# Performance work log

Hardware: AMD Instinct MI355X
Metric: run time of the kernel (lower is better)

Reference implementation:

```python
import jax, jax.numpy as jnp
import numpy as np

C_IN = 64
C_INT = 32

def conv1x1(x, w, b):
    # x: [B,C,H,W], w: [O,C], b: [O]
    return jnp.einsum('bchw,oc->bohw', x, w) + b[None, :, None, None]

def maxpool2(x):
    # 2x2 max pool, stride 2. x: [B,C,H,W]
    B, C, H, W = x.shape
    return x.reshape(B, C, H // 2, 2, W // 2, 2).max(axis=(3, 5))

def setup_inputs() -> dict:
    key = jax.random.key(0)
    ks = jax.random.split(key, 9)
    s = 1.0 / np.sqrt(C_IN)
    si = 1.0 / np.sqrt(C_INT)
    x = jax.random.normal(ks[0], (16, C_IN, 64, 64), dtype=jnp.float32)
    return {
        'x': x,
        'w_origin': jax.random.normal(ks[1], (C_INT, C_IN), dtype=jnp.float32) * s,
        'b_origin': jax.random.normal(ks[2], (C_INT,), dtype=jnp.float32) * s,
        'w_theta': jax.random.normal(ks[3], (C_INT, C_IN), dtype=jnp.float32) * s,
        'b_theta': jax.random.normal(ks[4], (C_INT,), dtype=jnp.float32) * s,
        'w_phi': jax.random.normal(ks[5], (C_INT, C_IN), dtype=jnp.float32) * s,
        'b_phi': jax.random.normal(ks[6], (C_INT,), dtype=jnp.float32) * s,
        'w_W': jax.random.normal(ks[7], (C_IN, C_INT), dtype=jnp.float32) * si,
        'b_W': jax.random.normal(ks[8], (C_IN,), dtype=jnp.float32) * si,
    }

def reference(x, w_origin, b_origin, w_theta, b_theta, w_phi, b_phi, w_W, b_W):
    B, C, H, W = x.shape
    # value: conv1x1 + maxpool -> [B, Ci, H/2, W/2] -> [B, Nkv, Ci]
    f_x = maxpool2(conv1x1(x, w_origin, b_origin))
    f_x = f_x.reshape(B, C_INT, -1).transpose(0, 2, 1)
    # query: conv1x1 (no pooling) -> [B, N, Ci]
    theta_x = conv1x1(x, w_theta, b_theta).reshape(B, C_INT, -1).transpose(0, 2, 1)
    # key: conv1x1 + maxpool -> [B, Ci, Nkv]
    phi_x = maxpool2(conv1x1(x, w_phi, b_phi)).reshape(B, C_INT, -1)
    # attention: [B, N, Nkv]
    f = jnp.einsum('bnc,bcm->bnm', theta_x, phi_x)
    f_div_C = jax.nn.softmax(f, axis=-1)
    y = jnp.einsum('bnm,bmc->bnc', f_div_C, f_x)  # [B, N, Ci]
    y = y.transpose(0, 2, 1).reshape(B, C_INT, H, W)
    z = conv1x1(y, w_W, b_W) + x
    return z
```

## Files before the change

### kernel.cpp

```cpp
#include <hip/hip_runtime.h>
#include <math.h>


#define B_SZ 16
#define HW 4096
#define NKV 1024
#define XSTR 65
#define YS 40
#define LOG2E 1.4426950408889634f

typedef __attribute__((ext_vector_type(8))) short bfrag;
typedef __attribute__((ext_vector_type(4))) short sfrag;
typedef __attribute__((ext_vector_type(4))) float f32x4;

static __device__ __forceinline__ ushort f2bf(float v) {
  union { float f; uint u; } c; c.f = v;
  uint b = c.u + 0x7FFFu + ((c.u >> 16) & 1u);
  return (ushort)(b >> 16);
}
static __device__ __forceinline__ float bf2f(ushort h) {
  union { uint u; float f; } c; c.u = (uint)h << 16; return c.f;
}
static __device__ __forceinline__ uint cvtpk(float a, float b) {
  uint r; asm("v_cvt_pk_bf16_f32 %0, %1, %2" : "=v"(r) : "v"(a), "v"(b));
  return r;
}
static __device__ __forceinline__ void split2(float a, float b, uint& h, uint& l) {
  h = cvtpk(a, b);
  float ha = __uint_as_float(h << 16);
  float hb = __uint_as_float(h & 0xFFFF0000u);
  l = cvtpk(a - ha, b - hb);
}

__global__ __launch_bounds__(256) void k_prep(
    const float* __restrict__ wt, const float* __restrict__ wp,
    const float* __restrict__ wo, const float* __restrict__ wW,
    ushort* __restrict__ WTH, ushort* __restrict__ WTL,
    ushort* __restrict__ WPH, ushort* __restrict__ WPL,
    ushort* __restrict__ WOH, ushort* __restrict__ WWH,
    ushort* __restrict__ WWL) {
  int t = threadIdx.x;
  int p = t >> 6, lane = t & 63, l15 = lane & 15, quad = lane >> 4;
  {
    int nt = p >> 1, kh2 = p & 1;
    const float* rt = wt + (size_t)(nt * 16 + l15) * 64 + kh2 * 32 + quad * 8;
    const float* rp = wp + (size_t)(nt * 16 + l15) * 64 + kh2 * 32 + quad * 8;
    const float* ro = wo + (size_t)(nt * 16 + l15) * 64 + kh2 * 32 + quad * 8;
    union { ushort u[8]; uint4 v; } th, tl, ph, pl, oh;
    #pragma unroll
    for (int j = 0; j < 8; ++j) {
      float v = rt[j] * LOG2E;
      ushort hb = f2bf(v);
      th.u[j] = hb; tl.u[j] = f2bf(v - bf2f(hb));
      v = rp[j]; hb = f2bf(v);
      ph.u[j] = hb; pl.u[j] = f2bf(v - bf2f(hb));
      oh.u[j] = f2bf(ro[j]);
    }
    size_t base = (size_t)t * 8;
    *(uint4*)(WTH + base) = th.v;
    *(uint4*)(WTL + base) = tl.v;
    *(uint4*)(WPH + base) = ph.v;
    *(uint4*)(WPL + base) = pl.v;
    *(uint4*)(WOH + base) = oh.v;
  }
  #pragma unroll
  for (int s = 0; s < 2; ++s) {
    int idx = s * 256 + t;
    int p2 = idx >> 6, ln = idx & 63;
    int fl = ln & 15, fq = ln >> 4;
    int wv = p2 >> 1, kt = p2 & 1;
    const float* rw = wW + (size_t)(wv * 16 + fl) * 32 + kt * 16 + fq * 4;
    union { ushort u[4]; uint2 v; } h, l;
    #pragma unroll
    for (int j = 0; j < 4; ++j) {
      float v = rw[j];
      ushort hb = f2bf(v);
      h.u[j] = hb; l.u[j] = f2bf(v - bf2f(hb));
    }
    *(uint2*)(WWH + (size_t)idx * 4) = h.v;
    *(uint2*)(WWL + (size_t)idx * 4) = l.v;
  }
}

__global__ __launch_bounds__(512) void k_qkv(
    const float* __restrict__ x,
    const ushort* __restrict__ WTH, const ushort* __restrict__ WTL,
    const float* __restrict__ bt,
    const ushort* __restrict__ WPH, const ushort* __restrict__ WPL,
    const float* __restrict__ bp,
    const ushort* __restrict__ WOH, const float* __restrict__ bo,
    ushort* __restrict__ QH, ushort* __restrict__ QL,
    ushort* __restrict__ KH, ushort* __restrict__ KL, ushort* __restrict__ VF) {
  __shared__ float sx[128 * XSTR];
  __shared__ float sPool[2][2][32][33];

  int t = threadIdx.x;
  int W = t >> 6, lane = t & 63, l15 = lane & 15, quad = lane >> 4;
  int bb = blockIdx.x >> 5, rg = blockIdx.x & 31;
  int p0 = rg * 128;

  #pragma unroll
  for (int i = 0; i < 4; ++i) {
    int f = i * 512 + t;
    int c = f >> 5, u = f & 31;
    float4 v = *(const float4*)(x + ((size_t)bb << 18) + (size_t)c * HW + p0 + 4 * u);
    sx[(4*u+0) * XSTR + c] = v.x;
    sx[(4*u+1) * XSTR + c] = v.y;
    sx[(4*u+2) * XSTR + c] = v.z;
    sx[(4*u+3) * XSTR + c] = v.w;
  }
  __syncthreads();

  int pix = W * 16 + l15;
  bfrag xh[2], xl[2];
  #pragma unroll
  for (int kh2 = 0; kh2 < 2; ++kh2) {
    union { uint u[4]; bfrag f; } H, L;
    #pragma unroll
    for (int jj = 0; jj < 4; ++jj) {
      float v0 = sx[pix * XSTR + kh2 * 32 + quad * 8 + 2 * jj];
      float v1 = sx[pix * XSTR + kh2 * 32 + quad * 8 + 2 * jj + 1];
      split2(v0, v1, H.u[jj], L.u[jj]);
    }
    xh[kh2] = H.f;
    xl[kh2] = L.f;
  }
  __syncthreads();

  f32x4 acc[2];

  acc[0] = (f32x4){0.f,0.f,0.f,0.f}; acc[1] = (f32x4){0.f,0.f,0.f,0.f};
  #pragma unroll
  for (int kh2 = 0; kh2 < 2; ++kh2)
    #pragma unroll
    for (int nt = 0; nt < 2; ++nt) {
      bfrag wh = *(const bfrag*)(WTH + ((size_t)(nt * 2 + kh2) * 64 + lane) * 8);
      bfrag wl = *(const bfrag*)(WTL + ((size_t)(nt * 2 + kh2) * 64 + lane) * 8);
      acc[nt] = __builtin_amdgcn_mfma_f32_16x16x32_bf16(xh[kh2], wh, acc[nt], 0, 0, 0);
      acc[nt] = __builtin_amdgcn_mfma_f32_16x16x32_bf16(xl[kh2], wh, acc[nt], 0, 0, 0);
      acc[nt] = __builtin_amdgcn_mfma_f32_16x16x32_bf16(xh[kh2], wl, acc[nt], 0, 0, 0);
    }
  #pragma unroll
  for (int nt = 0; nt < 2; ++nt) {
    float bias = bt[nt * 16 + l15] * LOG2E;
    #pragma unroll
    for (int r = 0; r < 4; ++r)
      sx[(W * 16 + quad * 4 + r) * XSTR + nt * 16 + l15] = acc[nt][r] + bias;
  }

  int prow = (W * 16 + quad * 4) >> 6;
  int px2  = ((W * 16 + quad * 4) & 63) >> 1;

  acc[0] = (f32x4){0.f,0.f,0.f,0.f}; acc[1] = (f32x4){0.f,0.f,0.f,0.f};
  #pragma unroll
  for (int kh2 = 0; kh2 < 2; ++kh2)
    #pragma unroll
    for (int nt = 0; nt < 2; ++nt) {
      bfrag wh = *(const bfrag*)(WPH + ((size_t)(nt * 2 + kh2) * 64 + lane) * 8);
      bfrag wl = *(const bfrag*)(WPL + ((size_t)(nt * 2 + kh2) * 64 + lane) * 8);
      acc[nt] = __builtin_amdgcn_mfma_f32_16x16x32_bf16(xh[kh2], wh, acc[nt], 0, 0, 0);
      acc[nt] = __builtin_amdgcn_mfma_f32_16x16x32_bf16(xl[kh2], wh, acc[nt], 0, 0, 0);
      acc[nt] = __builtin_amdgcn_mfma_f32_16x16x32_bf16(xh[kh2], wl, acc[nt], 0, 0, 0);
    }
  #pragma unroll
  for (int nt = 0; nt < 2; ++nt) {
    float bias = bp[nt * 16 + l15];
    sPool[0][prow][px2    ][nt * 16 + l15] = fmaxf(acc[nt][0], acc[nt][1]) + bias;
    sPool[0][prow][px2 + 1][nt * 16 + l15] = fmaxf(acc[nt][2], acc[nt][3]) + bias;
  }

  acc[0] = (f32x4){0.f,0.f,0.f,0.f}; acc[1] = (f32x4){0.f,0.f,0.f,0.f};
  #pragma unroll
  for (int kh2 = 0; kh2 < 2; ++kh2)
    #pragma unroll
    for (int nt = 0; nt < 2; ++nt) {
      bfrag wh = *(const bfrag*)(WOH + ((size_t)(nt * 2 + kh2) * 64 + lane) * 8);
      acc[nt] = __builtin_amdgcn_mfma_f32_16x16x32_bf16(xh[kh2], wh, acc[nt], 0, 0, 0);
      acc[nt] = __builtin_amdgcn_mfma_f32_16x16x32_bf16(xl[kh2], wh, acc[nt], 0, 0, 0);
    }
  #pragma unroll
  for (int nt = 0; nt < 2; ++nt) {
    float bias = bo[nt * 16 + l15];
    sPool[1][prow][px2    ][nt * 16 + l15] = fmaxf(acc[nt][0], acc[nt][1]) + bias;
    sPool[1][prow][px2 + 1][nt * 16 + l15] = fmaxf(acc[nt][2], acc[nt][3]) + bias;
  }
  __syncthreads();

  {
    int qt = t >> 6, ln = t & 63, fl = ln & 15, fq = ln >> 4;
    union { uint u[4]; uint4 v; } Hh, Ll;
    #pragma unroll
    for (int jj = 0; jj < 4; ++jj) {
      float v0 = sx[(qt * 16 + fl) * XSTR + fq * 8 + 2 * jj];
      float v1 = sx[(qt * 16 + fl) * XSTR + fq * 8 + 2 * jj + 1];
      split2(v0, v1, Hh.u[jj], Ll.u[jj]);
    }
    size_t base = ((size_t)(bb * 256 + rg * 8 + qt) * 64 + ln) * 8;
    *(uint4*)(QH + base) = Hh.v;
    *(uint4*)(QL + base) = Ll.v;
  }

  #pragma unroll
  for (int f = t; f < 1024; f += 512) {
    int tt = f >> 9, rem = f & 511;
    int ln = rem >> 3, j = rem & 7;
    int kvl = tt * 16 + (ln & 15);
    int ch = (ln >> 4) * 8 + j;
    float v = fmaxf(sPool[0][0][kvl][ch], sPool[0][1][kvl][ch]);
    ushort hb = f2bf(v);
    size_t base = ((size_t)(bb * 64 + rg * 2 + tt) * 64 + ln) * 8 + j;
    KH[base] = hb;
    KL[base] = f2bf(v - bf2f(hb));
  }

  #pragma unroll
  for (int f = t; f < 1024; f += 512) {
    int tt = f >> 9, mt = (f >> 8) & 1;
    int ln = (f >> 2) & 63, j = f & 3;
    int kvl = tt * 16 + ((ln >> 4) << 2) + j;
    int ch = mt * 16 + (ln & 15);
    float v = fmaxf(sPool[1][0][kvl][ch], sPool[1][1][kvl][ch]);
    VF[(((size_t)(bb * 64 + rg * 2 + tt) * 2 + mt) * 64 + ln) * 4 + j] = f2bf(v);
  }
}

__global__ __launch_bounds__(256, 4) void k_attn(
    const ushort* __restrict__ QH, const ushort* __restrict__ QL,
    const ushort* __restrict__ KH, const ushort* __restrict__ KL,
    const ushort* __restrict__ VF,
    const float* __restrict__ x,
    const ushort* __restrict__ WWH, const ushort* __restrict__ WWL,
    const float* __restrict__ bW, float* __restrict__ z) {
  __shared__ float smem[4 * 64 * 36 + 4 * 64];
  float* mrg = smem;
  float* sS  = smem + 4 * 64 * 36;

  int t = threadIdx.x;
  int w = t >> 6, lane = t & 63, l15 = lane & 15, quad = lane >> 4;
  int bb = blockIdx.x >> 6;
  int bq = blockIdx.x & 63;

  bfrag qh[4], ql[4];
  #pragma unroll
  for (int qt = 0; qt < 4; ++qt) {
    size_t base = ((size_t)(bb * 256 + bq * 4 + qt) * 64 + lane) * 8;
    qh[qt] = *(const bfrag*)(QH + base);
    ql[qt] = *(const bfrag*)(QL + base);
  }

  const ushort* KHb = KH + (size_t)bb * 64 * 64 * 8;
  const ushort* KLb = KL + (size_t)bb * 64 * 64 * 8;
  const ushort* VFb = VF + (size_t)bb * 64 * 2 * 64 * 4;

  f32x4 accO[4][2];
  float spart[4] = {0.f, 0.f, 0.f, 0.f};
  #pragma unroll
  for (int qt = 0; qt < 4; ++qt) {
    accO[qt][0] = (f32x4){0.f,0.f,0.f,0.f};
    accO[qt][1] = (f32x4){0.f,0.f,0.f,0.f};
  }

  bfrag kh[2], kl[2];
  sfrag vf[2][2];
  auto loadT = [&](int buf, int i) {
    int gt = w * 16 + i;
    size_t kb = ((size_t)gt * 64 + lane) * 8;
    kh[buf] = *(const bfrag*)(KHb + kb);
    kl[buf] = *(const bfrag*)(KLb + kb);
    vf[buf][0] = *(const sfrag*)(VFb + (((size_t)gt * 2 + 0) * 64 + lane) * 4);
    vf[buf][1] = *(const sfrag*)(VFb + (((size_t)gt * 2 + 1) * 64 + lane) * 4);
  };

  loadT(0, 0);
  #pragma unroll 2
  for (int i = 0; i < 16; ++i) {
    int cur = i & 1;
    if (i < 15) loadT(cur ^ 1, i + 1);
    __builtin_amdgcn_s_setprio(1);
    #pragma unroll
    for (int qt = 0; qt < 4; ++qt) {
      f32x4 s = (f32x4){0.f,0.f,0.f,0.f};
      s = __builtin_amdgcn_mfma_f32_16x16x32_bf16(kh[cur], qh[qt], s, 0, 0, 0);
      s = __builtin_amdgcn_mfma_f32_16x16x32_bf16(kh[cur], ql[qt], s, 0, 0, 0);
      s = __builtin_amdgcn_mfma_f32_16x16x32_bf16(kl[cur], qh[qt], s, 0, 0, 0);
      float e0 = exp2f(s[0]), e1 = exp2f(s[1]);
      float e2 = exp2f(s[2]), e3 = exp2f(s[3]);
      spart[qt] += (e0 + e1) + (e2 + e3);
      union { uint2 u; sfrag s4; } pk;
      pk.u.x = (__float_as_uint(e0) >> 16) | (__float_as_uint(e1) & 0xFFFF0000u);
      pk.u.y = (__float_as_uint(e2) >> 16) | (__float_as_uint(e3) & 0xFFFF0000u);
      accO[qt][0] = __builtin_amdgcn_mfma_f32_16x16x16bf16_1k(vf[cur][0], pk.s4, accO[qt][0], 0, 0, 0);
      accO[qt][1] = __builtin_amdgcn_mfma_f32_16x16x16bf16_1k(vf[cur][1], pk.s4, accO[qt][1], 0, 0, 0);
    }
    __builtin_amdgcn_s_setprio(0);
  }

  #pragma unroll
  for (int qt = 0; qt < 4; ++qt) {
    spart[qt] += __shfl_xor(spart[qt], 16);
    spart[qt] += __shfl_xor(spart[qt], 32);
  }

  #pragma unroll
  for (int qt = 0; qt < 4; ++qt) {
    #pragma unroll
    for (int mt = 0; mt < 2; ++mt)
      *(float4*)&mrg[((size_t)w * 64 + qt * 16 + l15) * 36 + mt * 16 + quad * 4] =
          make_float4(accO[qt][mt][0], accO[qt][mt][1], accO[qt][mt][2], accO[qt][mt][3]);
    if (lane < 16) sS[w * 64 + qt * 16 + l15] = spart[qt];
  }
  __syncthreads();

  int rq = t >> 2, rc = (t & 3) * 8;
  float yv[8];
  {
    float ssum = sS[rq] + sS[64 + rq] + sS[128 + rq] + sS[192 + rq];
    float inv = 1.0f / ssum;
    #pragma unroll
    for (int h = 0; h < 2; ++h) {
      float4 a = *(const float4*)&mrg[(size_t)rq * 36 + rc + 4 * h];
      float4 b = *(const float4*)&mrg[(size_t)(64 + rq) * 36 + rc + 4 * h];
      float4 c = *(const float4*)&mrg[(size_t)(128 + rq) * 36 + rc + 4 * h];
      float4 d = *(const float4*)&mrg[(size_t)(192 + rq) * 36 + rc + 4 * h];
      yv[4*h+0] = (a.x + b.x + c.x + d.x) * inv;
      yv[4*h+1] = (a.y + b.y + c.y + d.y) * inv;
      yv[4*h+2] = (a.z + b.z + c.z + d.z) * inv;
      yv[4*h+3] = (a.w + b.w + c.w + d.w) * inv;
    }
  }
  __syncthreads();

  ushort* yH = (ushort*)mrg;
  ushort* yL = yH + 64 * YS;
  {
    union { uint u[4]; uint4 v; } Hh, Ll;
    #pragma unroll
    for (int jj = 0; jj < 4; ++jj)
      split2(yv[2 * jj], yv[2 * jj + 1], Hh.u[jj], Ll.u[jj]);
    *(uint4*)&yH[rq * YS + rc] = Hh.v;
    *(uint4*)&yL[rq * YS + rc] = Ll.v;
  }
  __syncthreads();

  sfrag ah[2], al[2];
  #pragma unroll
  for (int kt = 0; kt < 2; ++kt) {
    ah[kt] = *(const sfrag*)(WWH + ((size_t)(w * 2 + kt) * 64 + lane) * 4);
    al[kt] = *(const sfrag*)(WWL + ((size_t)(w * 2 + kt) * 64 + lane) * 4);
  }
  #pragma unroll
  for (int nt = 0; nt < 4; ++nt) {
    f32x4 d = (f32x4){0.f,0.f,0.f,0.f};
    #pragma unroll
    for (int kt = 0; kt < 2; ++kt) {
      sfrag yhf = *(const sfrag*)&yH[(nt * 16 + l15) * YS + kt * 16 + quad * 4];
      sfrag ylf = *(const sfrag*)&yL[(nt * 16 + l15) * YS + kt * 16 + quad * 4];
      d = __builtin_amdgcn_mfma_f32_16x16x16bf16_1k(ah[kt], yhf, d, 0, 0, 0);
      d = __builtin_amdgcn_mfma_f32_16x16x16bf16_1k(al[kt], yhf, d, 0, 0, 0);
      d = __builtin_amdgcn_mfma_f32_16x16x16bf16_1k(ah[kt], ylf, d, 0, 0, 0);
    }
    #pragma unroll
    for (int r = 0; r < 4; ++r) {
      int cout = w * 16 + quad * 4 + r;
      size_t zi = ((size_t)bb << 18) + ((size_t)cout << 12)
                + (size_t)(bq * 4 + nt) * 16 + l15;
      z[zi] = d[r] + bW[cout] + x[zi];
    }
  }
}

extern "C" void kernel_launch(void* const* d_in, const int* in_sizes, int n_in,
                              void* d_out, int out_size, void* d_ws, size_t ws_size,
                              hipStream_t stream) {
  const float* x   = (const float*)d_in[0];
  const float* w_o = (const float*)d_in[1];
  const float* b_o = (const float*)d_in[2];
  const float* w_t = (const float*)d_in[3];
  const float* b_t = (const float*)d_in[4];
  const float* w_p = (const float*)d_in[5];
  const float* b_p = (const float*)d_in[6];
  const float* w_W = (const float*)d_in[7];
  const float* b_W = (const float*)d_in[8];
  float* z = (float*)d_out;

  ushort* QH = (ushort*)d_ws;
  ushort* QL = QH + 2097152;
  ushort* KH = QL + 2097152;
  ushort* KL = KH + 524288;
  ushort* VF = KL + 524288;
  ushort* WTH = VF + 524288;
  ushort* WTL = WTH + 2048;
  ushort* WPH = WTL + 2048;
  ushort* WPL = WPH + 2048;
  ushort* WOH = WPL + 2048;
  ushort* WWH = WOH + 2048;
  ushort* WWL = WWH + 2048;

  k_prep<<<dim3(1), dim3(256), 0, stream>>>(
      w_t, w_p, w_o, w_W, WTH, WTL, WPH, WPL, WOH, WWH, WWL);
  k_qkv<<<dim3(B_SZ * 32), dim3(512), 0, stream>>>(
      x, WTH, WTL, b_t, WPH, WPL, b_p, WOH, b_o, QH, QL, KH, KL, VF);
  k_attn<<<dim3(B_SZ * 64), dim3(256), 0, stream>>>(
      QH, QL, KH, KL, VF, x, WWH, WWL, b_W, z);
}
```

Measured before the change: 117.8 us.

## Compute query projection inside attention kernel instead of materializing Q

Moves the theta (query) 1x1 conv out of k_qkv and into k_attn: each attention block now loads its 64-pixel x tile into shared memory, runs the query MFMAs, and splits the result into hi/lo bf16 fragments in place. This drops the global write and reread of the QH/QL buffers (several MB per call). The residual x values are also prefetched into registers before the epilogue. In exchange, x is read twice (once in k_qkv, once in k_attn), k_attn gains extra syncs and a prologue, and register pressure rises under the 256x4 launch bounds.

```diff
diff --git a/kernel.cpp b/kernel.cpp
--- a/kernel.cpp
+++ b/kernel.cpp
@@ -84,12 +84,9 @@
 
 __global__ __launch_bounds__(512) void k_qkv(
     const float* __restrict__ x,
-    const ushort* __restrict__ WTH, const ushort* __restrict__ WTL,
-    const float* __restrict__ bt,
     const ushort* __restrict__ WPH, const ushort* __restrict__ WPL,
     const float* __restrict__ bp,
     const ushort* __restrict__ WOH, const float* __restrict__ bo,
-    ushort* __restrict__ QH, ushort* __restrict__ QL,
     ushort* __restrict__ KH, ushort* __restrict__ KL, ushort* __restrict__ VF) {
   __shared__ float sx[128 * XSTR];
   __shared__ float sPool[2][2][32][33];
@@ -125,31 +122,11 @@
     xh[kh2] = H.f;
     xl[kh2] = L.f;
   }
-  __syncthreads();
-
-  f32x4 acc[2];
-
-  acc[0] = (f32x4){0.f,0.f,0.f,0.f}; acc[1] = (f32x4){0.f,0.f,0.f,0.f};
-  #pragma unroll
-  for (int kh2 = 0; kh2 < 2; ++kh2)
-    #pragma unroll
-    for (int nt = 0; nt < 2; ++nt) {
-      bfrag wh = *(const bfrag*)(WTH + ((size_t)(nt * 2 + kh2) * 64 + lane) * 8);
-      bfrag wl = *(const bfrag*)(WTL + ((size_t)(nt * 2 + kh2) * 64 + lane) * 8);
-      acc[nt] = __builtin_amdgcn_mfma_f32_16x16x32_bf16(xh[kh2], wh, acc[nt], 0, 0, 0);
-      acc[nt] = __builtin_amdgcn_mfma_f32_16x16x32_bf16(xl[kh2], wh, acc[nt], 0, 0, 0);
-      acc[nt] = __builtin_amdgcn_mfma_f32_16x16x32_bf16(xh[kh2], wl, acc[nt], 0, 0, 0);
-    }
-  #pragma unroll
-  for (int nt = 0; nt < 2; ++nt) {
-    float bias = bt[nt * 16 + l15] * LOG2E;
-    #pragma unroll
-    for (int r = 0; r < 4; ++r)
-      sx[(W * 16 + quad * 4 + r) * XSTR + nt * 16 + l15] = acc[nt][r] + bias;
-  }
 
   int prow = (W * 16 + quad * 4) >> 6;
   int px2  = ((W * 16 + quad * 4) & 63) >> 1;
+
+  f32x4 acc[2];
 
   acc[0] = (f32x4){0.f,0.f,0.f,0.f}; acc[1] = (f32x4){0.f,0.f,0.f,0.f};
   #pragma unroll
@@ -185,20 +162,6 @@
     sPool[1][prow][px2 + 1][nt * 16 + l15] = fmaxf(acc[nt][2], acc[nt][3]) + bias;
   }
   __syncthreads();
-
-  {
-    int qt = t >> 6, ln = t & 63, fl = ln & 15, fq = ln >> 4;
-    union { uint u[4]; uint4 v; } Hh, Ll;
-    #pragma unroll
-    for (int jj = 0; jj < 4; ++jj) {
-      float v0 = sx[(qt * 16 + fl) * XSTR + fq * 8 + 2 * jj];
-      float v1 = sx[(qt * 16 + fl) * XSTR + fq * 8 + 2 * jj + 1];
-      split2(v0, v1, Hh.u[jj], Ll.u[jj]);
-    }
-    size_t base = ((size_t)(bb * 256 + rg * 8 + qt) * 64 + ln) * 8;
-    *(uint4*)(QH + base) = Hh.v;
-    *(uint4*)(QL + base) = Ll.v;
-  }
 
   #pragma unroll
   for (int f = t; f < 1024; f += 512) {
@@ -225,28 +188,89 @@
 }
 
 __global__ __launch_bounds__(256, 4) void k_attn(
-    const ushort* __restrict__ QH, const ushort* __restrict__ QL,
     const ushort* __restrict__ KH, const ushort* __restrict__ KL,
     const ushort* __restrict__ VF,
+    const ushort* __restrict__ WTH, const ushort* __restrict__ WTL,
+    const float* __restrict__ bt,
     const float* __restrict__ x,
     const ushort* __restrict__ WWH, const ushort* __restrict__ WWL,
     const float* __restrict__ bW, float* __restrict__ z) {
   __shared__ float smem[4 * 64 * 36 + 4 * 64];
   float* mrg = smem;
   float* sS  = smem + 4 * 64 * 36;
+  float* sxa = smem;
+  float* sth = smem + 64 * 65;
 
   int t = threadIdx.x;
   int w = t >> 6, lane = t & 63, l15 = lane & 15, quad = lane >> 4;
   int bb = blockIdx.x >> 6;
   int bq = blockIdx.x & 63;
+  int p0 = bq * 64;
+
+  #pragma unroll
+  for (int i = 0; i < 4; ++i) {
+    int f = i * 256 + t;
+    int c = f >> 4, u = (f & 15) * 4;
+    float4 v = *(const float4*)(x + ((size_t)bb << 18) + (size_t)c * HW + p0 + u);
+    sxa[(u+0) * 65 + c] = v.x;
+    sxa[(u+1) * 65 + c] = v.y;
+    sxa[(u+2) * 65 + c] = v.z;
+    sxa[(u+3) * 65 + c] = v.w;
+  }
+  __syncthreads();
+
+  int pix = w * 16 + l15;
+  bfrag xh[2], xl[2];
+  #pragma unroll
+  for (int kh2 = 0; kh2 < 2; ++kh2) {
+    union { uint u[4]; bfrag f; } H, L;
+    #pragma unroll
+    for (int jj = 0; jj < 4; ++jj) {
+      float v0 = sxa[pix * 65 + kh2 * 32 + quad * 8 + 2 * jj];
+      float v1 = sxa[pix * 65 + kh2 * 32 + quad * 8 + 2 * jj + 1];
+      split2(v0, v1, H.u[jj], L.u[jj]);
+    }
+    xh[kh2] = H.f;
+    xl[kh2] = L.f;
+  }
+
+  {
+    f32x4 acc[2];
+    acc[0] = (f32x4){0.f,0.f,0.f,0.f}; acc[1] = (f32x4){0.f,0.f,0.f,0.f};
+    #pragma unroll
+    for (int kh2 = 0; kh2 < 2; ++kh2)
+      #pragma unroll
+      for (int nt = 0; nt < 2; ++nt) {
+        bfrag wh = *(const bfrag*)(WTH + ((size_t)(nt * 2 + kh2) * 64 + lane) * 8);
+        bfrag wl = *(const bfrag*)(WTL + ((size_t)(nt * 2 + kh2) * 64 + lane) * 8);
+        acc[nt] = __builtin_amdgcn_mfma_f32_16x16x32_bf16(xh[kh2], wh, acc[nt], 0, 0, 0);
+        acc[nt] = __builtin_amdgcn_mfma_f32_16x16x32_bf16(xl[kh2], wh, acc[nt], 0, 0, 0);
+        acc[nt] = __builtin_amdgcn_mfma_f32_16x16x32_bf16(xh[kh2], wl, acc[nt], 0, 0, 0);
+      }
+    #pragma unroll
+    for (int nt = 0; nt < 2; ++nt) {
+      float bias = bt[nt * 16 + l15] * LOG2E;
+      #pragma unroll
+      for (int r = 0; r < 4; ++r)
+        sth[(w * 16 + quad * 4 + r) * 33 + nt * 16 + l15] = acc[nt][r] + bias;
+    }
+  }
+  __syncthreads();
 
   bfrag qh[4], ql[4];
   #pragma unroll
   for (int qt = 0; qt < 4; ++qt) {
-    size_t base = ((size_t)(bb * 256 + bq * 4 + qt) * 64 + lane) * 8;
-    qh[qt] = *(const bfrag*)(QH + base);
-    ql[qt] = *(const bfrag*)(QL + base);
-  }
+    union { uint u[4]; bfrag f; } H, L;
+    #pragma unroll
+    for (int jj = 0; jj < 4; ++jj) {
+      float v0 = sth[(qt * 16 + l15) * 33 + quad * 8 + 2 * jj];
+      float v1 = sth[(qt * 16 + l15) * 33 + quad * 8 + 2 * jj + 1];
+      split2(v0, v1, H.u[jj], L.u[jj]);
+    }
+    qh[qt] = H.f;
+    ql[qt] = L.f;
+  }
+  __syncthreads();
 
   const ushort* KHb = KH + (size_t)bb * 64 * 64 * 8;
   const ushort* KLb = KL + (size_t)bb * 64 * 64 * 8;
@@ -295,6 +319,16 @@
     __builtin_amdgcn_s_setprio(0);
   }
 
+  float xres[4][4];
+  #pragma unroll
+  for (int nt = 0; nt < 4; ++nt)
+    #pragma unroll
+    for (int r = 0; r < 4; ++r) {
+      int cout = w * 16 + quad * 4 + r;
+      xres[nt][r] = x[((size_t)bb << 18) + ((size_t)cout << 12)
+                    + (size_t)(bq * 4 + nt) * 16 + l15];
+    }
+
   #pragma unroll
   for (int qt = 0; qt < 4; ++qt) {
     spart[qt] += __shfl_xor(spart[qt], 16);
@@ -364,7 +398,7 @@
       int cout = w * 16 + quad * 4 + r;
       size_t zi = ((size_t)bb << 18) + ((size_t)cout << 12)
                 + (size_t)(bq * 4 + nt) * 16 + l15;
-      z[zi] = d[r] + bW[cout] + x[zi];
+      z[zi] = d[r] + bW[cout] + xres[nt][r];
     }
   }
 }
@@ -383,9 +417,7 @@
   const float* b_W = (const float*)d_in[8];
   float* z = (float*)d_out;
 
-  ushort* QH = (ushort*)d_ws;
-  ushort* QL = QH + 2097152;
-  ushort* KH = QL + 2097152;
+  ushort* KH = (ushort*)d_ws;
   ushort* KL = KH + 524288;
   ushort* VF = KL + 524288;
   ushort* WTH = VF + 524288;
@@ -399,7 +431,7 @@
   k_prep<<<dim3(1), dim3(256), 0, stream>>>(
       w_t, w_p, w_o, w_W, WTH, WTL, WPH, WPL, WOH, WWH, WWL);
   k_qkv<<<dim3(B_SZ * 32), dim3(512), 0, stream>>>(
-      x, WTH, WTL, b_t, WPH, WPL, b_p, WOH, b_o, QH, QL, KH, KL, VF);
+      x, WPH, WPL, b_p, WOH, b_o, KH, KL, VF);
   k_attn<<<dim3(B_SZ * 64), dim3(256), 0, stream>>>(
-      QH, QL, KH, KL, VF, x, WWH, WWL, b_W, z);
-}
+      KH, KL, VF, WTH, WTL, b_t, x, WWH, WWL, b_W, z);
+}
```

New measurement: 119.3 us. About the same (+1.2%).
